# Performance work log

Measured on AMD Instinct MI355X. Metric: run time of the kernel, lower is better.

## Reference

```python
import jax, jax.numpy as jnp
import numpy as np

BASE = 10000.0

def positional_encoding(seq_len, dim, dtype=jnp.float32):
    # standard sinusoidal PE: pe[p, 2i] = sin(p / BASE^(2i/dim)), pe[p, 2i+1] = cos(...)
    pos = jnp.arange(seq_len, dtype=dtype)[:, None]            # [S,1]
    idx = jnp.arange(0, dim, 2, dtype=dtype)[None, :]          # [1,dim/2]
    ang = pos / jnp.power(BASE, idx / dim)                     # [S,dim/2]
    pe = jnp.zeros((seq_len, dim), dtype=dtype)
    pe = pe.at[:, 0::2].set(jnp.sin(ang)).at[:, 1::2].set(jnp.cos(ang))
    return pe

def setup_inputs() -> dict:
    key = jax.random.key(0)
    ks = jax.random.split(key, 5)
    B, S, H, D = 16, 2048, 128, 64
    x = jax.random.normal(ks[0], (B, S, H), dtype=jnp.float32)
    Wq = jax.random.normal(ks[1], (H, D), dtype=jnp.float32) * (H ** -0.5)
    Wk = jax.random.normal(ks[2], (H, D), dtype=jnp.float32) * (H ** -0.5)
    Wv = jax.random.normal(ks[3], (H, D), dtype=jnp.float32) * (H ** -0.5)
    Wf = jax.random.normal(ks[4], (D, 1), dtype=jnp.float32) * (D ** -0.5)
    bf = jnp.zeros((1,), dtype=jnp.float32)
    return {"x": x, "Wq": Wq, "Wk": Wk, "Wv": Wv, "Wf": Wf, "bf": bf}

def reference(x, Wq, Wk, Wv, Wf, bf):
    B, S, H = x.shape
    xp = x + positional_encoding(S, H, x.dtype)[None]          # add PE, broadcast over batch
    Q = jnp.einsum('bsh,hd->bsd', xp, Wq)
    K = jnp.einsum('bsh,hd->bsd', xp, Wk)
    V = jnp.einsum('bsh,hd->bsd', xp, Wv)
    D = K.shape[-1]
    scores = jnp.einsum('bqd,bkd->bqk', Q, K) / jnp.sqrt(jnp.asarray(D, x.dtype))
    # NOTE: softmax over dim=1 (the QUERY axis), per the original nn.Softmax(dim=1)
    attn = jax.nn.softmax(scores, axis=1)                      # [B,S,S]
    z = jnp.einsum('bqk,bkd->bqd', attn, V)                    # [B,S,D]
    out = (jnp.einsum('bsd,do->bso', z, Wf) + bf).squeeze(-1)  # [B,S]
    return out
```

## Files before the change

### kernel.cpp

```cpp
#include <hip/hip_runtime.h>
#include <hip/hip_bf16.h>
#include <math.h>

#define BATCH 16
#define SEQ   2048
#define HID   128
#define DIM   64

typedef __attribute__((ext_vector_type(8))) short bf16x8;
typedef __attribute__((ext_vector_type(4))) float f32x4;

#define QSCALE 0.18033688011112042f
#define C0_PE  0.07195578314043169f

static __device__ __forceinline__ ushort f2bf(float f) {
    union { float f; unsigned u; } v; v.f = f;
    unsigned r = v.u + 0x7FFFu + ((v.u >> 16) & 1u);
    return (ushort)(r >> 16);
}

static __device__ __forceinline__ float fast_exp2(float x) {
#if __has_builtin(__builtin_amdgcn_exp2f)
    return __builtin_amdgcn_exp2f(x);
#else
    return exp2f(x);
#endif
}

__global__ void k_prep(const float* __restrict__ Wq, const float* __restrict__ Wk,
                       const float* __restrict__ Wv, const float* __restrict__ Wf,
                       ushort* __restrict__ Wt, float* __restrict__ wvf) {
    const int tid = threadIdx.x;
    if (tid < HID) {
        float s = 0.f;
        #pragma unroll 8
        for (int d = 0; d < DIM; ++d) s += Wv[tid * DIM + d] * Wf[d];
        wvf[tid] = s;
    }
    for (int i = tid; i < 128 * 128; i += 256) {
        int col = i >> 7, k = i & 127;
        float v = (col < 64) ? Wq[k * DIM + col] * QSCALE : Wk[k * DIM + (col - 64)];
        Wt[i] = f2bf(v);
    }
}

__global__ __launch_bounds__(256) void k_qkv(
    const float* __restrict__ x, const ushort* __restrict__ Wt,
    const float* __restrict__ wvf, ushort* __restrict__ Qb,
    ushort* __restrict__ Kb, float* __restrict__ vf)
{
    const int tid  = threadIdx.x;
    const int wave = tid >> 6;
    const int lane = tid & 63;
    const int quad = lane >> 4;
    const int col  = lane & 15;
    const int rowbase = blockIdx.x * 64 + wave * 16;
    const int grow = rowbase + col;
    const float pos = (float)(grow & (SEQ - 1));

    bf16x8 af[4];
    float vpart = 0.f;
    #pragma unroll
    for (int c = 0; c < 4; ++c) {
        const float* xp = x + (size_t)grow * HID + quad * 8 + c * 32;
        float4 v0 = *(const float4*)(xp);
        float4 v1 = *(const float4*)(xp + 4);
        float t[8] = {v0.x, v0.y, v0.z, v0.w, v1.x, v1.y, v1.z, v1.w};
        #pragma unroll
        for (int jp = 0; jp < 4; ++jp) {
            int h = quad * 8 + c * 32 + jp * 2;
            float ang = pos * __expf(-(float)h * C0_PE);
            t[jp * 2]     += __sinf(ang);
            t[jp * 2 + 1] += __cosf(ang);
        }
        const float* wp = wvf + quad * 8 + c * 32;
        float4 w0 = *(const float4*)(wp);
        float4 w1 = *(const float4*)(wp + 4);
        vpart += t[0] * w0.x + t[1] * w0.y + t[2] * w0.z + t[3] * w0.w +
                 t[4] * w1.x + t[5] * w1.y + t[6] * w1.z + t[7] * w1.w;
        short* ap = (short*)&af[c];
        #pragma unroll
        for (int j = 0; j < 8; ++j) ap[j] = (short)f2bf(t[j]);
    }

    vpart += __shfl_xor(vpart, 16);
    vpart += __shfl_xor(vpart, 32);
    if (quad == 0) vf[grow] = vpart;

    #pragma unroll
    for (int t = 0; t < 8; ++t) {
        const ushort* wrow = Wt + (size_t)(t * 16 + col) * 128 + quad * 8;
        f32x4 acc = {0.f, 0.f, 0.f, 0.f};
        #pragma unroll
        for (int c = 0; c < 4; ++c) {
            bf16x8 bfr = *(const bf16x8*)(wrow + c * 32);
            acc = __builtin_amdgcn_mfma_f32_16x16x32_bf16(af[c], bfr, acc, 0, 0, 0);
        }
        const int cb = (t & 3) * 16 + col;
        ushort* dst = (t < 4) ? Qb : Kb;
        const int r0 = rowbase + quad * 4;
        #pragma unroll
        for (int r = 0; r < 4; ++r)
            dst[(size_t)(r0 + r) * DIM + cb] = f2bf(acc[r]);
    }
}

__global__ __launch_bounds__(512) void k_attn(
    const ushort* __restrict__ Qb, const ushort* __restrict__ Kb,
    const float* __restrict__ vf, const float* __restrict__ bfp,
    float* __restrict__ outp)
{
    const int b    = blockIdx.y;
    const int k0   = blockIdx.x * 64;
    const int tid  = threadIdx.x;
    const int wave = tid >> 6;
    const int lane = tid & 63;
    const int quad = lane >> 4;
    const int col  = lane & 15;

    __shared__ float sl[8][64];
    __shared__ float wcol[64];

    bf16x8 kf[4][2];
    {
        const ushort* Kbase = Kb + ((size_t)(b * SEQ + k0)) * DIM;
        #pragma unroll
        for (int t = 0; t < 4; ++t)
            #pragma unroll
            for (int c = 0; c < 2; ++c)
                kf[t][c] = *(const bf16x8*)(Kbase + (size_t)(t * 16 + col) * DIM + quad * 8 + c * 32);
    }

    const ushort* Qstart = Qb + ((size_t)(b * SEQ + wave * 256 + col)) * DIM + quad * 8;

    float l[4] = {0.f, 0.f, 0.f, 0.f};
    {
        const ushort* Qrow = Qstart;
        for (int qi = 0; qi < 16; ++qi) {
            bf16x8 a0 = *(const bf16x8*)(Qrow);
            bf16x8 a1 = *(const bf16x8*)(Qrow + 32);
            Qrow += 16 * DIM;
            #pragma unroll
            for (int t = 0; t < 4; ++t) {
                f32x4 acc = {0.f, 0.f, 0.f, 0.f};
                acc = __builtin_amdgcn_mfma_f32_16x16x32_bf16(a0, kf[t][0], acc, 0, 0, 0);
                acc = __builtin_amdgcn_mfma_f32_16x16x32_bf16(a1, kf[t][1], acc, 0, 0, 0);
                l[t] += fast_exp2(acc.x) + fast_exp2(acc.y) +
                        fast_exp2(acc.z) + fast_exp2(acc.w);
            }
        }
    }
    #pragma unroll
    for (int t = 0; t < 4; ++t) {
        l[t] += __shfl_xor(l[t], 16);
        l[t] += __shfl_xor(l[t], 32);
    }
    if (quad == 0) {
        #pragma unroll
        for (int t = 0; t < 4; ++t) sl[wave][t * 16 + col] = l[t];
    }
    __syncthreads();
    if (tid < 64) {
        float ll = 0.f;
        #pragma unroll
        for (int w = 0; w < 8; ++w) ll += sl[w][tid];
        wcol[tid] = vf[(size_t)b * SEQ + k0 + tid] / ll;
    }
    __syncthreads();

    const float bias = bfp[0] * (1.0f / (SEQ / 64));
    float wreg[4];
    #pragma unroll
    for (int t = 0; t < 4; ++t) wreg[t] = wcol[t * 16 + col];

    {
        const ushort* Qrow = Qstart;
        float* outb = outp + (size_t)b * SEQ;
        for (int qi = 0; qi < 16; ++qi) {
            bf16x8 a0 = *(const bf16x8*)(Qrow);
            bf16x8 a1 = *(const bf16x8*)(Qrow + 32);
            Qrow += 16 * DIM;
            float rs[4] = {0.f, 0.f, 0.f, 0.f};
            #pragma unroll
            for (int t = 0; t < 4; ++t) {
                f32x4 acc = {0.f, 0.f, 0.f, 0.f};
                acc = __builtin_amdgcn_mfma_f32_16x16x32_bf16(a0, kf[t][0], acc, 0, 0, 0);
                acc = __builtin_amdgcn_mfma_f32_16x16x32_bf16(a1, kf[t][1], acc, 0, 0, 0);
                #pragma unroll
                for (int r = 0; r < 4; ++r)
                    rs[r] += fast_exp2(acc[r]) * wreg[t];
            }
            #pragma unroll
            for (int r = 0; r < 4; ++r) {
                float v = rs[r];
                v += __shfl_xor(v, 1); v += __shfl_xor(v, 2);
                v += __shfl_xor(v, 4); v += __shfl_xor(v, 8);
                rs[r] = v;
            }
            if (col == 0) {
                const int qrow = wave * 256 + qi * 16 + quad * 4;
                #pragma unroll
                for (int r = 0; r < 4; ++r)
                    atomicAdd(&outb[qrow + r], rs[r] + bias);
            }
        }
    }
}

extern "C" void kernel_launch(void* const* d_in, const int* in_sizes, int n_in,
                              void* d_out, int out_size, void* d_ws, size_t ws_size,
                              hipStream_t stream) {
    (void)in_sizes; (void)n_in; (void)ws_size;
    const float* x  = (const float*)d_in[0];
    const float* Wq = (const float*)d_in[1];
    const float* Wk = (const float*)d_in[2];
    const float* Wv = (const float*)d_in[3];
    const float* Wf = (const float*)d_in[4];
    const float* bf = (const float*)d_in[5];
    float* outp = (float*)d_out;

    float*  wvf = (float*)d_ws;
    float*  vf  = wvf + 256;
    ushort* Wt  = (ushort*)(vf + (size_t)BATCH * SEQ);
    ushort* Qb  = Wt + 128 * 128;
    ushort* Kb  = Qb + (size_t)BATCH * SEQ * DIM;

    hipMemsetAsync(d_out, 0, (size_t)out_size * sizeof(float), stream);
    k_prep<<<1, 256, 0, stream>>>(Wq, Wk, Wv, Wf, Wt, wvf);
    k_qkv<<<BATCH * SEQ / 64, 256, 0, stream>>>(x, Wt, wvf, Qb, Kb, vf);
    k_attn<<<dim3(SEQ / 64, BATCH), 512, 0, stream>>>(Qb, Kb, vf, bf, outp);
}
```

Baseline: 136.5 us.

## Split attention into column-sum and row-sum kernels over query chunks

Splits the single attention kernel into two launches: one computes partial softmax column sums per query chunk into a workspace buffer, and the other reduces those partials and accumulates the weighted row sums. The query axis is split into four chunks, giving four times as many smaller blocks. This is meant to raise occupancy and CU load balance. The cost is an extra launch, reloading K fragments, and extra global traffic for the partial sums.

```diff
diff --git a/kernel.cpp b/kernel.cpp
--- a/kernel.cpp
+++ b/kernel.cpp
@@ -6,6 +6,7 @@
 #define SEQ   2048
 #define HID   128
 #define DIM   64
+#define QCH   4
 
 typedef __attribute__((ext_vector_type(8))) short bf16x8;
 typedef __attribute__((ext_vector_type(4))) float f32x4;
@@ -105,21 +106,20 @@
     }
 }
 
-__global__ __launch_bounds__(512) void k_attn(
+__global__ __launch_bounds__(256, 6) void k_colsum(
     const ushort* __restrict__ Qb, const ushort* __restrict__ Kb,
-    const float* __restrict__ vf, const float* __restrict__ bfp,
-    float* __restrict__ outp)
+    float* __restrict__ lpart)
 {
     const int b    = blockIdx.y;
     const int k0   = blockIdx.x * 64;
+    const int qc   = blockIdx.z;
     const int tid  = threadIdx.x;
     const int wave = tid >> 6;
     const int lane = tid & 63;
     const int quad = lane >> 4;
     const int col  = lane & 15;
 
-    __shared__ float sl[8][64];
-    __shared__ float wcol[64];
+    __shared__ float sl[4][64];
 
     bf16x8 kf[4][2];
     {
@@ -131,23 +131,21 @@
                 kf[t][c] = *(const bf16x8*)(Kbase + (size_t)(t * 16 + col) * DIM + quad * 8 + c * 32);
     }
 
-    const ushort* Qstart = Qb + ((size_t)(b * SEQ + wave * 256 + col)) * DIM + quad * 8;
+    const ushort* Qrow = Qb +
+        ((size_t)(b * SEQ + qc * (SEQ / QCH) + wave * 128 + col)) * DIM + quad * 8;
 
     float l[4] = {0.f, 0.f, 0.f, 0.f};
-    {
-        const ushort* Qrow = Qstart;
-        for (int qi = 0; qi < 16; ++qi) {
-            bf16x8 a0 = *(const bf16x8*)(Qrow);
-            bf16x8 a1 = *(const bf16x8*)(Qrow + 32);
-            Qrow += 16 * DIM;
-            #pragma unroll
-            for (int t = 0; t < 4; ++t) {
-                f32x4 acc = {0.f, 0.f, 0.f, 0.f};
-                acc = __builtin_amdgcn_mfma_f32_16x16x32_bf16(a0, kf[t][0], acc, 0, 0, 0);
-                acc = __builtin_amdgcn_mfma_f32_16x16x32_bf16(a1, kf[t][1], acc, 0, 0, 0);
-                l[t] += fast_exp2(acc.x) + fast_exp2(acc.y) +
-                        fast_exp2(acc.z) + fast_exp2(acc.w);
-            }
+    for (int qi = 0; qi < 8; ++qi) {
+        bf16x8 a0 = *(const bf16x8*)(Qrow);
+        bf16x8 a1 = *(const bf16x8*)(Qrow + 32);
+        Qrow += 16 * DIM;
+        #pragma unroll
+        for (int t = 0; t < 4; ++t) {
+            f32x4 acc = {0.f, 0.f, 0.f, 0.f};
+            acc = __builtin_amdgcn_mfma_f32_16x16x32_bf16(a0, kf[t][0], acc, 0, 0, 0);
+            acc = __builtin_amdgcn_mfma_f32_16x16x32_bf16(a1, kf[t][1], acc, 0, 0, 0);
+            l[t] += fast_exp2(acc.x) + fast_exp2(acc.y) +
+                    fast_exp2(acc.z) + fast_exp2(acc.w);
         }
     }
     #pragma unroll
@@ -161,9 +159,42 @@
     }
     __syncthreads();
     if (tid < 64) {
+        float ll = sl[0][tid] + sl[1][tid] + sl[2][tid] + sl[3][tid];
+        lpart[((size_t)qc * BATCH + b) * SEQ + k0 + tid] = ll;
+    }
+}
+
+__global__ __launch_bounds__(256, 6) void k_rowsum(
+    const ushort* __restrict__ Qb, const ushort* __restrict__ Kb,
+    const float* __restrict__ vf, const float* __restrict__ lpart,
+    const float* __restrict__ bfp, float* __restrict__ outp)
+{
+    const int b    = blockIdx.y;
+    const int k0   = blockIdx.x * 64;
+    const int qc   = blockIdx.z;
+    const int tid  = threadIdx.x;
+    const int wave = tid >> 6;
+    const int lane = tid & 63;
+    const int quad = lane >> 4;
+    const int col  = lane & 15;
+
+    __shared__ float wcol[64];
+
+    bf16x8 kf[4][2];
+    {
+        const ushort* Kbase = Kb + ((size_t)(b * SEQ + k0)) * DIM;
+        #pragma unroll
+        for (int t = 0; t < 4; ++t)
+            #pragma unroll
+            for (int c = 0; c < 2; ++c)
+                kf[t][c] = *(const bf16x8*)(Kbase + (size_t)(t * 16 + col) * DIM + quad * 8 + c * 32);
+    }
+
+    if (tid < 64) {
         float ll = 0.f;
         #pragma unroll
-        for (int w = 0; w < 8; ++w) ll += sl[w][tid];
+        for (int q = 0; q < QCH; ++q)
+            ll += lpart[((size_t)q * BATCH + b) * SEQ + k0 + tid];
         wcol[tid] = vf[(size_t)b * SEQ + k0 + tid] / ll;
     }
     __syncthreads();
@@ -173,36 +204,36 @@
     #pragma unroll
     for (int t = 0; t < 4; ++t) wreg[t] = wcol[t * 16 + col];
 
-    {
-        const ushort* Qrow = Qstart;
-        float* outb = outp + (size_t)b * SEQ;
-        for (int qi = 0; qi < 16; ++qi) {
-            bf16x8 a0 = *(const bf16x8*)(Qrow);
-            bf16x8 a1 = *(const bf16x8*)(Qrow + 32);
-            Qrow += 16 * DIM;
-            float rs[4] = {0.f, 0.f, 0.f, 0.f};
-            #pragma unroll
-            for (int t = 0; t < 4; ++t) {
-                f32x4 acc = {0.f, 0.f, 0.f, 0.f};
-                acc = __builtin_amdgcn_mfma_f32_16x16x32_bf16(a0, kf[t][0], acc, 0, 0, 0);
-                acc = __builtin_amdgcn_mfma_f32_16x16x32_bf16(a1, kf[t][1], acc, 0, 0, 0);
-                #pragma unroll
-                for (int r = 0; r < 4; ++r)
-                    rs[r] += fast_exp2(acc[r]) * wreg[t];
-            }
-            #pragma unroll
-            for (int r = 0; r < 4; ++r) {
-                float v = rs[r];
-                v += __shfl_xor(v, 1); v += __shfl_xor(v, 2);
-                v += __shfl_xor(v, 4); v += __shfl_xor(v, 8);
-                rs[r] = v;
-            }
-            if (col == 0) {
-                const int qrow = wave * 256 + qi * 16 + quad * 4;
-                #pragma unroll
-                for (int r = 0; r < 4; ++r)
-                    atomicAdd(&outb[qrow + r], rs[r] + bias);
-            }
+    const ushort* Qrow = Qb +
+        ((size_t)(b * SEQ + qc * (SEQ / QCH) + wave * 128 + col)) * DIM + quad * 8;
+    float* outb = outp + (size_t)b * SEQ;
+
+    for (int qi = 0; qi < 8; ++qi) {
+        bf16x8 a0 = *(const bf16x8*)(Qrow);
+        bf16x8 a1 = *(const bf16x8*)(Qrow + 32);
+        Qrow += 16 * DIM;
+        float rs[4] = {0.f, 0.f, 0.f, 0.f};
+        #pragma unroll
+        for (int t = 0; t < 4; ++t) {
+            f32x4 acc = {0.f, 0.f, 0.f, 0.f};
+            acc = __builtin_amdgcn_mfma_f32_16x16x32_bf16(a0, kf[t][0], acc, 0, 0, 0);
+            acc = __builtin_amdgcn_mfma_f32_16x16x32_bf16(a1, kf[t][1], acc, 0, 0, 0);
+            #pragma unroll
+            for (int r = 0; r < 4; ++r)
+                rs[r] += fast_exp2(acc[r]) * wreg[t];
+        }
+        #pragma unroll
+        for (int r = 0; r < 4; ++r) {
+            float v = rs[r];
+            v += __shfl_xor(v, 1); v += __shfl_xor(v, 2);
+            v += __shfl_xor(v, 4); v += __shfl_xor(v, 8);
+            rs[r] = v;
+        }
+        if (col == 0) {
+            const int qrow = qc * (SEQ / QCH) + wave * 128 + qi * 16 + quad * 4;
+            #pragma unroll
+            for (int r = 0; r < 4; ++r)
+                atomicAdd(&outb[qrow + r], rs[r] + bias);
         }
     }
 }
@@ -224,9 +255,11 @@
     ushort* Wt  = (ushort*)(vf + (size_t)BATCH * SEQ);
     ushort* Qb  = Wt + 128 * 128;
     ushort* Kb  = Qb + (size_t)BATCH * SEQ * DIM;
+    float*  lpart = (float*)(Kb + (size_t)BATCH * SEQ * DIM);
 
     hipMemsetAsync(d_out, 0, (size_t)out_size * sizeof(float), stream);
     k_prep<<<1, 256, 0, stream>>>(Wq, Wk, Wv, Wf, Wt, wvf);
     k_qkv<<<BATCH * SEQ / 64, 256, 0, stream>>>(x, Wt, wvf, Qb, Kb, vf);
-    k_attn<<<dim3(SEQ / 64, BATCH), 512, 0, stream>>>(Qb, Kb, vf, bf, outp);
-}
+    k_colsum<<<dim3(SEQ / 64, BATCH, QCH), 256, 0, stream>>>(Qb, Kb, lpart);
+    k_rowsum<<<dim3(SEQ / 64, BATCH, QCH), 256, 0, stream>>>(Qb, Kb, vf, lpart, bf, outp);
+}
```

Result: slower. 158.0 us (+15.8%).
